# Performance work log

Measured on AMD Instinct MI355X. Metric: run time of the kernel, lower is better.

Reference implementation:

```python
import jax, jax.numpy as jnp
import numpy as np

S = 1024      # MAX_SEQ_LEN
D_IN = 4096
H = 32        # num_heads
G = 8         # num_kv_groups
HD = 128      # head_dim
GS = H // G   # group_size


def _rope(t, cos, sin):
    # t: [heads, S, HD]; cos/sin: [S, HD]
    half = HD // 2
    t1, t2 = t[..., :half], t[..., half:]
    rotated = jnp.concatenate([-t2, t1], axis=-1)
    return t * cos[None] + rotated * sin[None]


def setup_inputs() -> dict:
    key = jax.random.key(0)
    ks = jax.random.split(key, 8)
    x = jax.random.normal(ks[0], (1, S, D_IN), dtype=jnp.float32)
    mask = jnp.triu(jnp.ones((S, S), dtype=bool), k=1)  # causal: True above diagonal
    # RoPE tables (standard llama frequencies)
    inv_freq = 1.0 / (10000.0 ** (jnp.arange(0, HD, 2, dtype=jnp.float32) / HD))
    angles = jnp.arange(S, dtype=jnp.float32)[:, None] * inv_freq[None, :]  # [S, HD/2]
    angles = jnp.concatenate([angles, angles], axis=-1)                     # [S, HD]
    cos, sin = jnp.cos(angles), jnp.sin(angles)
    sc = 0.02
    Wq = jax.random.normal(ks[1], (D_IN, H * HD), dtype=jnp.float32) * sc
    Wk = jax.random.normal(ks[2], (D_IN, G * HD), dtype=jnp.float32) * sc
    Wv = jax.random.normal(ks[3], (D_IN, G * HD), dtype=jnp.float32) * sc
    Wo = jax.random.normal(ks[4], (H * HD, D_IN), dtype=jnp.float32) * sc
    return {"x": x, "mask": mask, "cos": cos, "sin": sin,
            "Wq": Wq, "Wk": Wk, "Wv": Wv, "Wo": Wo}


def reference(x, mask, cos, sin, Wq, Wk, Wv, Wo):
    b, n_tok, _ = x.shape  # b == 1 (module squeezes dim 0)
    xs = x[0]                                        # [S, d_in]
    q = (xs @ Wq).reshape(n_tok, H, HD).transpose(1, 0, 2)   # [H, S, HD]
    k = (xs @ Wk).reshape(n_tok, G, HD).transpose(1, 0, 2)   # [G, S, HD]
    v = (xs @ Wv).reshape(n_tok, G, HD).transpose(1, 0, 2)   # [G, S, HD]
    q = _rope(q, cos, sin)
    k = _rope(k, cos, sin)
    # GQA expansion: repeat_interleave over head dim
    k = jnp.repeat(k, GS, axis=0)                    # [H, S, HD]
    v = jnp.repeat(v, GS, axis=0)
    scores = jnp.einsum('hsd,htd->hst', q, k)        # [H, S, S]
    scores = jnp.where(mask[None], -jnp.inf, scores) / jnp.sqrt(jnp.float32(HD))
    weights = jax.nn.softmax(scores, axis=-1)
    ctx = jnp.einsum('hst,htd->hsd', weights, v)     # [H, S, HD]
    ctx = ctx.transpose(1, 0, 2).reshape(n_tok, H * HD)
    out = ctx @ Wo                                   # [S, d_in]
    return out[None]                                 # [1, S, d_in]
```

## Files before the change

### kernel.cpp

```cpp
#include <hip/hip_runtime.h>
#include <hip/hip_bf16.h>

#define S_LEN 1024
#define DIN 4096
#define NH 32
#define NG 8
#define HD 128

typedef __bf16 bf16x8 __attribute__((ext_vector_type(8)));
typedef __bf16 bf16x4 __attribute__((ext_vector_type(4)));
typedef float f32x4 __attribute__((ext_vector_type(4)));

__device__ __forceinline__ void gload_lds16(const void* g, void* l) {
  __builtin_amdgcn_global_load_lds(
      (const __attribute__((address_space(1))) unsigned int*)g,
      (__attribute__((address_space(3))) unsigned int*)l, 16, 0, 0);
}

__device__ __forceinline__ unsigned pack2bf(float a, float b) {
  union { __bf16 h[2]; unsigned u; } x;
  x.h[0] = (__bf16)a; x.h[1] = (__bf16)b;
  return x.u;
}

__global__ __launch_bounds__(256) void k_cast(const float* __restrict__ in,
                                              __bf16* __restrict__ out, int n4) {
  int i = blockIdx.x * 256 + threadIdx.x;
  if (i >= n4) return;
  const float4 v = ((const float4*)in)[i];
  bf16x4 o;
  o.x = (__bf16)v.x; o.y = (__bf16)v.y; o.z = (__bf16)v.z; o.w = (__bf16)v.w;
  ((bf16x4*)out)[i] = o;
}

__global__ __launch_bounds__(256) void k_transpose_cast(const float* __restrict__ W,
                                                        __bf16* __restrict__ WT,
                                                        int N, int K) {
  __shared__ __bf16 t[64][80];
  const int tid = threadIdx.x;
  const int k0 = blockIdx.y * 64, n0 = blockIdx.x * 64;
#pragma unroll
  for (int p = 0; p < 4; ++p) {
    int kk = p * 16 + (tid >> 4);
    int nn = (tid & 15) * 4;
    const float4 v = *(const float4*)&W[(size_t)(k0 + kk) * N + n0 + nn];
    t[nn + 0][kk] = (__bf16)v.x;
    t[nn + 1][kk] = (__bf16)v.y;
    t[nn + 2][kk] = (__bf16)v.z;
    t[nn + 3][kk] = (__bf16)v.w;
  }
  __syncthreads();
#pragma unroll
  for (int p = 0; p < 2; ++p) {
    int nn = p * 32 + (tid >> 3);
    int kk = (tid & 7) * 8;
    bf16x8 v = *(const bf16x8*)&t[nn][kk];
    *(bf16x8*)&WT[(size_t)(n0 + nn) * K + k0 + kk] = v;
  }
}

__global__ __launch_bounds__(256) void k_rope(__bf16* __restrict__ Q, __bf16* __restrict__ Kb,
                                              const float* __restrict__ cosT,
                                              const float* __restrict__ sinT) {
  int idx = blockIdx.x * 256 + threadIdx.x;
  const int QP = S_LEN * NH * 64;
  __bf16* t; int nh;
  if (idx < QP) { t = Q; nh = NH; }
  else {
    idx -= QP; t = Kb; nh = NG;
    if (idx >= S_LEN * NG * 64) return;
  }
  int d = idx & 63;
  int h = (idx >> 6) % nh;
  int s = idx / (64 * nh);
  float c = cosT[s * HD + d], sn = sinT[s * HD + d];
  size_t base = (size_t)s * nh * HD + h * HD + d;
  float t1 = (float)t[base], t2 = (float)t[base + 64];
  t[base]      = (__bf16)(t1 * c - t2 * sn);
  t[base + 64] = (__bf16)(t2 * c + t1 * sn);
}

__global__ __launch_bounds__(256) void k_vt(const __bf16* __restrict__ V,
                                            __bf16* __restrict__ Vt) {
  __shared__ __bf16 t[64][72];
  const int tid = threadIdx.x;
  const int s0 = blockIdx.y * 64, d0 = blockIdx.x * 64;
#pragma unroll
  for (int p = 0; p < 2; ++p) {
    int ss = p * 32 + (tid >> 3);
    int dd = (tid & 7) * 8;
    bf16x8 v = *(const bf16x8*)&V[(size_t)(s0 + ss) * 1024 + d0 + dd];
#pragma unroll
    for (int e = 0; e < 8; ++e) t[dd + e][ss] = v[e];
  }
  __syncthreads();
#pragma unroll
  for (int p = 0; p < 2; ++p) {
    int dd = p * 32 + (tid >> 3);
    int ss = (tid & 7) * 8;
    *(bf16x8*)&Vt[(size_t)(d0 + dd) * 1024 + s0 + ss] = *(const bf16x8*)&t[dd][ss];
  }
}

template <int MODE, typename OutT>
__global__ __launch_bounds__(256, 3) void k_gemm(const __bf16* __restrict__ A,
                                                 const __bf16* __restrict__ Bt,
                                                 OutT* __restrict__ C, int N, int K,
                                                 __bf16* __restrict__ Qb,
                                                 __bf16* __restrict__ Kb,
                                                 __bf16* __restrict__ Vb) {
  __shared__ __bf16 As[128 * 64], Bs[64 * 64];
  const int bm = blockIdx.y, bn = blockIdx.x;
  const int tid = threadIdx.x, w = tid >> 6;
  const int l = tid & 63, l15 = l & 15, g4 = l >> 4;

  f32x4 acc[2][4];
#pragma unroll
  for (int i = 0; i < 2; ++i)
#pragma unroll
    for (int j = 0; j < 4; ++j)
#pragma unroll
      for (int r = 0; r < 4; ++r) acc[i][j][r] = 0.f;

  for (int k0 = 0; k0 < K; k0 += 64) {
#pragma unroll
    for (int p = 0; p < 4; ++p) {
      int c = p * 256 + tid;
      int row = c >> 3, gc = (c & 7) ^ (row & 7);
      gload_lds16(&A[(size_t)(bm * 128 + row) * K + k0 + gc * 8], &As[(p * 256 + w * 64) * 8]);
    }
#pragma unroll
    for (int p = 0; p < 2; ++p) {
      int c = p * 256 + tid;
      int row = c >> 3, gc = (c & 7) ^ (row & 7);
      gload_lds16(&Bt[(size_t)(bn * 64 + row) * K + k0 + gc * 8], &Bs[(p * 256 + w * 64) * 8]);
    }
    __syncthreads();

    bf16x8 af[2][2], bfr[4][2];
#pragma unroll
    for (int i = 0; i < 2; ++i) {
      int m = w * 32 + i * 16 + l15;
#pragma unroll
      for (int kk = 0; kk < 2; ++kk)
        af[i][kk] = *(const bf16x8*)((const char*)As + m * 128 + (((kk * 4 + g4) ^ (m & 7)) << 4));
    }
#pragma unroll
    for (int j = 0; j < 4; ++j) {
      int n = j * 16 + l15;
#pragma unroll
      for (int kk = 0; kk < 2; ++kk)
        bfr[j][kk] = *(const bf16x8*)((const char*)Bs + n * 128 + (((kk * 4 + g4) ^ (n & 7)) << 4));
    }
#pragma unroll
    for (int kk = 0; kk < 2; ++kk)
#pragma unroll
      for (int i = 0; i < 2; ++i)
#pragma unroll
        for (int j = 0; j < 4; ++j)
          acc[i][j] = __builtin_amdgcn_mfma_f32_16x16x32_bf16(af[i][kk], bfr[j][kk], acc[i][j], 0, 0, 0);
    __syncthreads();
  }

  if constexpr (MODE == 0) {
#pragma unroll
    for (int i = 0; i < 2; ++i)
#pragma unroll
      for (int j = 0; j < 4; ++j)
#pragma unroll
        for (int r = 0; r < 4; ++r) {
          size_t row = bm * 128 + w * 32 + i * 16 + g4 * 4 + r;
          size_t col = bn * 64 + j * 16 + l15;
          C[row * N + col] = (OutT)acc[i][j][r];
        }
  } else {
    const int nb0 = bn * 64;
    __bf16* dst; int ldc, coff;
    if (nb0 < 4096)      { dst = Qb; ldc = 4096; coff = 0; }
    else if (nb0 < 5120) { dst = Kb; ldc = 1024; coff = 4096; }
    else                 { dst = Vb; ldc = 1024; coff = 5120; }
#pragma unroll
    for (int i = 0; i < 2; ++i)
#pragma unroll
      for (int j = 0; j < 4; ++j)
#pragma unroll
        for (int r = 0; r < 4; ++r) {
          size_t row = bm * 128 + w * 32 + i * 16 + g4 * 4 + r;
          size_t col = nb0 + j * 16 + l15 - coff;
          dst[row * ldc + col] = (__bf16)acc[i][j][r];
        }
  }
}

__global__ __launch_bounds__(256) void k_attn(const __bf16* __restrict__ Q,
                                              const __bf16* __restrict__ Kb,
                                              const __bf16* __restrict__ Vt,
                                              __bf16* __restrict__ ctx) {
  __shared__ __align__(16) char lds_raw[65536];
  __bf16* Ks = (__bf16*)lds_raw;
  __bf16* Vs = (__bf16*)(lds_raw + 32768);

  const int h = blockIdx.y, g = h >> 2;
  const int q0 = blockIdx.x * 64;
  const int tid = threadIdx.x, w = tid >> 6, l = tid & 63;
  const int l15 = l & 15, g4 = l >> 4;
  const float scale = 0.08838834764831845f;

  bf16x8 qf[4];
  const int qrow = q0 + w * 16 + l15;
#pragma unroll
  for (int ks = 0; ks < 4; ++ks)
    qf[ks] = *(const bf16x8*)&Q[(size_t)qrow * (NH * HD) + h * HD + ks * 32 + g4 * 8];

  f32x4 acc[8];
#pragma unroll
  for (int i = 0; i < 8; ++i)
#pragma unroll
    for (int r = 0; r < 4; ++r) acc[i][r] = 0.f;
  float m_run = -__builtin_inff(), l_run = 0.f;

  const int ntiles = (q0 + 64 + 127) >> 7;
  for (int kt = 0; kt < ntiles; ++kt) {
    const int kv0 = kt * 128;
#pragma unroll
    for (int p = 0; p < 8; ++p) {
      int c = p * 256 + tid;
      int row = c >> 4, cc = c & 15;
      gload_lds16(&Kb[(size_t)(kv0 + row) * (NG * HD) + g * HD + ((cc ^ (row & 7)) << 3)],
                  &Ks[(p * 256 + w * 64) * 8]);
      gload_lds16(&Vt[(size_t)(g * HD + row) * S_LEN + kv0 + ((cc ^ (row & 7)) << 3)],
                  &Vs[(p * 256 + w * 64) * 8]);
    }
    __syncthreads();

    float sreg[8][4];
    const bool need_mask = (kv0 + 127 > q0);
#pragma unroll
    for (int tf = 0; tf < 8; ++tf) {
      f32x4 sa;
#pragma unroll
      for (int r = 0; r < 4; ++r) sa[r] = 0.f;
      int t_loc = tf * 16 + l15;
#pragma unroll
      for (int ks = 0; ks < 4; ++ks) {
        bf16x8 kf = *(const bf16x8*)((const char*)Ks + t_loc * 256 + (((ks * 4 + g4) ^ (t_loc & 7)) << 4));
        sa = __builtin_amdgcn_mfma_f32_16x16x32_bf16(kf, qf[ks], sa, 0, 0, 0);
      }
#pragma unroll
      for (int r = 0; r < 4; ++r) {
        float v = sa[r] * scale;
        if (need_mask && (kv0 + tf * 16 + g4 * 4 + r) > qrow) v = -__builtin_inff();
        sreg[tf][r] = v;
      }
    }
    float mx = -__builtin_inff();
#pragma unroll
    for (int tf = 0; tf < 8; ++tf)
#pragma unroll
      for (int r = 0; r < 4; ++r) mx = fmaxf(mx, sreg[tf][r]);
    mx = fmaxf(mx, __shfl_xor(mx, 16));
    mx = fmaxf(mx, __shfl_xor(mx, 32));
    const float m_new = fmaxf(m_run, mx);
    const float alpha = __expf(m_run - m_new);
    float ssum = 0.f;
#pragma unroll
    for (int tf = 0; tf < 8; ++tf)
#pragma unroll
      for (int r = 0; r < 4; ++r) {
        sreg[tf][r] = __expf(sreg[tf][r] - m_new);
        ssum += sreg[tf][r];
      }
    ssum += __shfl_xor(ssum, 16);
    ssum += __shfl_xor(ssum, 32);
    l_run = l_run * alpha + ssum;
    m_run = m_new;
    float ar[4];
#pragma unroll
    for (int r = 0; r < 4; ++r) ar[r] = __shfl(alpha, g4 * 4 + r);
#pragma unroll
    for (int nf = 0; nf < 8; ++nf)
#pragma unroll
      for (int r = 0; r < 4; ++r) acc[nf][r] *= ar[r];

    __syncthreads();

    char* pb = lds_raw + w * 4096;
#pragma unroll
    for (int tf = 0; tf < 8; ++tf) {
      int chunkc = 2 * tf + (g4 >> 1);
      int addr = l15 * 256 + ((chunkc ^ (l15 & 7)) << 4) + ((g4 & 1) << 3);
      *(unsigned*)(pb + addr)     = pack2bf(sreg[tf][0], sreg[tf][1]);
      *(unsigned*)(pb + addr + 4) = pack2bf(sreg[tf][2], sreg[tf][3]);
    }
    asm volatile("s_waitcnt lgkmcnt(0)" ::: "memory");
    bf16x8 pf[4];
#pragma unroll
    for (int ks = 0; ks < 4; ++ks)
      pf[ks] = *(const bf16x8*)(pb + l15 * 256 + (((ks * 4 + g4) ^ (l15 & 7)) << 4));
#pragma unroll
    for (int nf = 0; nf < 8; ++nf) {
      int d_loc = nf * 16 + l15;
#pragma unroll
      for (int ks = 0; ks < 4; ++ks) {
        bf16x8 vf = *(const bf16x8*)((const char*)Vs + d_loc * 256 + (((ks * 4 + g4) ^ (d_loc & 7)) << 4));
        acc[nf] = __builtin_amdgcn_mfma_f32_16x16x32_bf16(pf[ks], vf, acc[nf], 0, 0, 0);
      }
    }
    __syncthreads();
  }
  float li[4];
#pragma unroll
  for (int r = 0; r < 4; ++r) li[r] = 1.f / __shfl(l_run, g4 * 4 + r);
#pragma unroll
  for (int nf = 0; nf < 8; ++nf)
#pragma unroll
    for (int r = 0; r < 4; ++r) {
      size_t row = q0 + w * 16 + g4 * 4 + r;
      size_t col = (size_t)h * HD + nf * 16 + l15;
      ctx[row * (NH * HD) + col] = (__bf16)(acc[nf][r] * li[r]);
    }
}

extern "C" void kernel_launch(void* const* d_in, const int* in_sizes, int n_in,
                              void* d_out, int out_size, void* d_ws, size_t ws_size,
                              hipStream_t stream) {
  const float* x    = (const float*)d_in[0];
  const float* cosT = (const float*)d_in[2];
  const float* sinT = (const float*)d_in[3];
  const float* Wq   = (const float*)d_in[4];
  const float* Wk   = (const float*)d_in[5];
  const float* Wv   = (const float*)d_in[6];
  const float* Wo   = (const float*)d_in[7];
  float* out = (float*)d_out;

  char* ws = (char*)d_ws;
  const size_t MB = 1u << 20;
  __bf16* xb    = (__bf16*)(ws + 0);
  __bf16* WqkvT = (__bf16*)(ws + 8 * MB);
  __bf16* WoT   = (__bf16*)(ws + 56 * MB);
  __bf16* Qb    = (__bf16*)(ws + 88 * MB);
  __bf16* Kbuf  = (__bf16*)(ws + 96 * MB);
  __bf16* Vb    = (__bf16*)(ws + 98 * MB);
  __bf16* Vtb   = (__bf16*)(ws + 100 * MB);
  __bf16* ctxb  = (__bf16*)(ws + 0);

  k_cast<<<4096, 256, 0, stream>>>(x, xb, (S_LEN * DIN) / 4);
  k_transpose_cast<<<dim3(64, 64), 256, 0, stream>>>(Wq, WqkvT, 4096, 4096);
  k_transpose_cast<<<dim3(16, 64), 256, 0, stream>>>(Wk, WqkvT + (size_t)4096 * 4096, 1024, 4096);
  k_transpose_cast<<<dim3(16, 64), 256, 0, stream>>>(Wv, WqkvT + (size_t)5120 * 4096, 1024, 4096);
  k_transpose_cast<<<dim3(64, 64), 256, 0, stream>>>(Wo, WoT, 4096, 4096);

  k_gemm<1, __bf16><<<dim3(96, 8), 256, 0, stream>>>(xb, WqkvT, (__bf16*)nullptr, 6144, 4096,
                                                     Qb, Kbuf, Vb);
  k_rope<<<10240, 256, 0, stream>>>(Qb, Kbuf, cosT, sinT);
  k_vt<<<dim3(16, 16), 256, 0, stream>>>(Vb, Vtb);

  k_attn<<<dim3(16, 32), 256, 0, stream>>>(Qb, Kbuf, Vtb, ctxb);

  k_gemm<0, float><<<dim3(64, 8), 256, 0, stream>>>(ctxb, WoT, out, 4096, 4096,
                                                    nullptr, nullptr, nullptr);
}
```

Baseline: 223.2 us.

## Merge prep kernels, double-buffer GEMM LDS, fuse V transpose, vectorize RoPE

Folds the x cast and the four weight transpose-casts into one launch, and double-buffers the GEMM's LDS tiles so the next K-tile loads while the current one is computed. The QKV GEMM epilogue writes V straight into transposed layout, which removes the separate transpose kernel. RoPE now processes four elements per thread with vector loads. Together these cut launch count and exposed load latency, at the cost of twice the LDS per GEMM block, which may lower occupancy.

```diff
diff --git a/kernel.cpp b/kernel.cpp
--- a/kernel.cpp
+++ b/kernel.cpp
@@ -23,22 +23,33 @@
   return x.u;
 }
 
-__global__ __launch_bounds__(256) void k_cast(const float* __restrict__ in,
-                                              __bf16* __restrict__ out, int n4) {
-  int i = blockIdx.x * 256 + threadIdx.x;
-  if (i >= n4) return;
-  const float4 v = ((const float4*)in)[i];
-  bf16x4 o;
-  o.x = (__bf16)v.x; o.y = (__bf16)v.y; o.z = (__bf16)v.z; o.w = (__bf16)v.w;
-  ((bf16x4*)out)[i] = o;
-}
-
-__global__ __launch_bounds__(256) void k_transpose_cast(const float* __restrict__ W,
-                                                        __bf16* __restrict__ WT,
-                                                        int N, int K) {
+__global__ __launch_bounds__(256) void k_prep(const float* __restrict__ x,
+                                              const float* __restrict__ Wq,
+                                              const float* __restrict__ Wk,
+                                              const float* __restrict__ Wv,
+                                              const float* __restrict__ Wo,
+                                              __bf16* __restrict__ xb,
+                                              __bf16* __restrict__ WqkvT,
+                                              __bf16* __restrict__ WoT) {
   __shared__ __bf16 t[64][80];
   const int tid = threadIdx.x;
-  const int k0 = blockIdx.y * 64, n0 = blockIdx.x * 64;
+  int bid = blockIdx.x;
+  if (bid < 4096) {
+    int i = bid * 256 + tid;
+    const float4 v = ((const float4*)x)[i];
+    bf16x4 o;
+    o.x = (__bf16)v.x; o.y = (__bf16)v.y; o.z = (__bf16)v.z; o.w = (__bf16)v.w;
+    ((bf16x4*)xb)[i] = o;
+    return;
+  }
+  bid -= 4096;
+  const float* W; __bf16* WT; int N, off, tau;
+  if (bid < 4096)       { W = Wq; WT = WqkvT; N = 4096; off = 0;    tau = bid; }
+  else if (bid < 5120)  { W = Wk; WT = WqkvT; N = 1024; off = 4096; tau = bid - 4096; }
+  else if (bid < 6144)  { W = Wv; WT = WqkvT; N = 1024; off = 5120; tau = bid - 5120; }
+  else                  { W = Wo; WT = WoT;   N = 4096; off = 0;    tau = bid - 6144; }
+  const int ntx = N >> 6;
+  const int n0 = (tau % ntx) * 64, k0 = (tau / ntx) * 64;
 #pragma unroll
   for (int p = 0; p < 4; ++p) {
     int kk = p * 16 + (tid >> 4);
@@ -55,7 +66,7 @@
     int nn = p * 32 + (tid >> 3);
     int kk = (tid & 7) * 8;
     bf16x8 v = *(const bf16x8*)&t[nn][kk];
-    *(bf16x8*)&WT[(size_t)(n0 + nn) * K + k0 + kk] = v;
+    *(bf16x8*)&WT[(size_t)(off + n0 + nn) * DIN + k0 + kk] = v;
   }
 }
 
@@ -63,57 +74,46 @@
                                               const float* __restrict__ cosT,
                                               const float* __restrict__ sinT) {
   int idx = blockIdx.x * 256 + threadIdx.x;
-  const int QP = S_LEN * NH * 64;
-  __bf16* t; int nh;
-  if (idx < QP) { t = Q; nh = NH; }
-  else {
-    idx -= QP; t = Kb; nh = NG;
-    if (idx >= S_LEN * NG * 64) return;
-  }
-  int d = idx & 63;
-  int h = (idx >> 6) % nh;
-  int s = idx / (64 * nh);
-  float c = cosT[s * HD + d], sn = sinT[s * HD + d];
-  size_t base = (size_t)s * nh * HD + h * HD + d;
-  float t1 = (float)t[base], t2 = (float)t[base + 64];
-  t[base]      = (__bf16)(t1 * c - t2 * sn);
-  t[base + 64] = (__bf16)(t2 * c + t1 * sn);
-}
-
-__global__ __launch_bounds__(256) void k_vt(const __bf16* __restrict__ V,
-                                            __bf16* __restrict__ Vt) {
-  __shared__ __bf16 t[64][72];
-  const int tid = threadIdx.x;
-  const int s0 = blockIdx.y * 64, d0 = blockIdx.x * 64;
-#pragma unroll
-  for (int p = 0; p < 2; ++p) {
-    int ss = p * 32 + (tid >> 3);
-    int dd = (tid & 7) * 8;
-    bf16x8 v = *(const bf16x8*)&V[(size_t)(s0 + ss) * 1024 + d0 + dd];
-#pragma unroll
-    for (int e = 0; e < 8; ++e) t[dd + e][ss] = v[e];
-  }
-  __syncthreads();
-#pragma unroll
-  for (int p = 0; p < 2; ++p) {
-    int dd = p * 32 + (tid >> 3);
-    int ss = (tid & 7) * 8;
-    *(bf16x8*)&Vt[(size_t)(d0 + dd) * 1024 + s0 + ss] = *(const bf16x8*)&t[dd][ss];
-  }
-}
-
-template <int MODE, typename OutT>
+  int d = (idx & 15) * 4;
+  int row = idx >> 4;
+  __bf16* p; int s;
+  if (row < S_LEN * NH) { p = Q + (size_t)row * HD; s = row >> 5; }
+  else { int r = row - S_LEN * NH; p = Kb + (size_t)r * HD; s = r >> 3; }
+  const float4 c = *(const float4*)&cosT[s * HD + d];
+  const float4 sn = *(const float4*)&sinT[s * HD + d];
+  bf16x4 a = *(const bf16x4*)&p[d];
+  bf16x4 b = *(const bf16x4*)&p[d + 64];
+  bf16x4 oa, ob;
+  oa.x = (__bf16)((float)a.x * c.x - (float)b.x * sn.x);
+  oa.y = (__bf16)((float)a.y * c.y - (float)b.y * sn.y);
+  oa.z = (__bf16)((float)a.z * c.z - (float)b.z * sn.z);
+  oa.w = (__bf16)((float)a.w * c.w - (float)b.w * sn.w);
+  ob.x = (__bf16)((float)b.x * c.x + (float)a.x * sn.x);
+  ob.y = (__bf16)((float)b.y * c.y + (float)a.y * sn.y);
+  ob.z = (__bf16)((float)b.z * c.z + (float)a.z * sn.z);
+  ob.w = (__bf16)((float)b.w * c.w + (float)a.w * sn.w);
+  *(bf16x4*)&p[d] = oa;
+  *(bf16x4*)&p[d + 64] = ob;
+}
+
+template <int MODE>
 __global__ __launch_bounds__(256, 3) void k_gemm(const __bf16* __restrict__ A,
                                                  const __bf16* __restrict__ Bt,
-                                                 OutT* __restrict__ C, int N, int K,
+                                                 float* __restrict__ C,
                                                  __bf16* __restrict__ Qb,
                                                  __bf16* __restrict__ Kb,
-                                                 __bf16* __restrict__ Vb) {
-  __shared__ __bf16 As[128 * 64], Bs[64 * 64];
+                                                 __bf16* __restrict__ Vt) {
+  __shared__ __bf16 As[2][128 * 64];
+  __shared__ __bf16 Bs[2][64 * 64];
   const int bm = blockIdx.y, bn = blockIdx.x;
+  const int K = DIN, NT = K / 64;
+
   const int tid = threadIdx.x, w = tid >> 6;
   const int l = tid & 63, l15 = l & 15, g4 = l >> 4;
 
+  const __bf16* Asrc = A + (size_t)(bm * 128) * K;
+  const __bf16* Bsrc = Bt + (size_t)(bn * 64) * K;
+
   f32x4 acc[2][4];
 #pragma unroll
   for (int i = 0; i < 2; ++i)
@@ -122,35 +122,37 @@
 #pragma unroll
       for (int r = 0; r < 4; ++r) acc[i][j][r] = 0.f;
 
-  for (int k0 = 0; k0 < K; k0 += 64) {
+  auto issueA = [&](int t, __bf16* dst) {
 #pragma unroll
     for (int p = 0; p < 4; ++p) {
       int c = p * 256 + tid;
       int row = c >> 3, gc = (c & 7) ^ (row & 7);
-      gload_lds16(&A[(size_t)(bm * 128 + row) * K + k0 + gc * 8], &As[(p * 256 + w * 64) * 8]);
-    }
+      gload_lds16(Asrc + (size_t)row * K + t * 64 + gc * 8, dst + (p * 256 + w * 64) * 8);
+    }
+  };
+  auto issueB = [&](int t, __bf16* dst) {
 #pragma unroll
     for (int p = 0; p < 2; ++p) {
       int c = p * 256 + tid;
       int row = c >> 3, gc = (c & 7) ^ (row & 7);
-      gload_lds16(&Bt[(size_t)(bn * 64 + row) * K + k0 + gc * 8], &Bs[(p * 256 + w * 64) * 8]);
-    }
-    __syncthreads();
-
+      gload_lds16(Bsrc + (size_t)row * K + t * 64 + gc * 8, dst + (p * 256 + w * 64) * 8);
+    }
+  };
+  auto compute = [&](const __bf16* Ab, const __bf16* Bb) {
     bf16x8 af[2][2], bfr[4][2];
 #pragma unroll
     for (int i = 0; i < 2; ++i) {
       int m = w * 32 + i * 16 + l15;
 #pragma unroll
       for (int kk = 0; kk < 2; ++kk)
-        af[i][kk] = *(const bf16x8*)((const char*)As + m * 128 + (((kk * 4 + g4) ^ (m & 7)) << 4));
+        af[i][kk] = *(const bf16x8*)((const char*)Ab + m * 128 + (((kk * 4 + g4) ^ (m & 7)) << 4));
     }
 #pragma unroll
     for (int j = 0; j < 4; ++j) {
       int n = j * 16 + l15;
 #pragma unroll
       for (int kk = 0; kk < 2; ++kk)
-        bfr[j][kk] = *(const bf16x8*)((const char*)Bs + n * 128 + (((kk * 4 + g4) ^ (n & 7)) << 4));
+        bfr[j][kk] = *(const bf16x8*)((const char*)Bb + n * 128 + (((kk * 4 + g4) ^ (n & 7)) << 4));
     }
 #pragma unroll
     for (int kk = 0; kk < 2; ++kk)
@@ -159,6 +161,17 @@
 #pragma unroll
         for (int j = 0; j < 4; ++j)
           acc[i][j] = __builtin_amdgcn_mfma_f32_16x16x32_bf16(af[i][kk], bfr[j][kk], acc[i][j], 0, 0, 0);
+  };
+
+  issueA(0, As[0]); issueB(0, Bs[0]);
+  __syncthreads();
+
+  for (int t = 0; t < NT; t += 2) {
+    issueA(t + 1, As[1]); issueB(t + 1, Bs[1]);
+    compute(As[0], Bs[0]);
+    __syncthreads();
+    if (t + 2 < NT) { issueA(t + 2, As[0]); issueB(t + 2, Bs[0]); }
+    compute(As[1], Bs[1]);
     __syncthreads();
   }
 
@@ -171,24 +184,37 @@
         for (int r = 0; r < 4; ++r) {
           size_t row = bm * 128 + w * 32 + i * 16 + g4 * 4 + r;
           size_t col = bn * 64 + j * 16 + l15;
-          C[row * N + col] = (OutT)acc[i][j][r];
+          C[row * 4096 + col] = acc[i][j][r];
         }
   } else {
     const int nb0 = bn * 64;
-    __bf16* dst; int ldc, coff;
-    if (nb0 < 4096)      { dst = Qb; ldc = 4096; coff = 0; }
-    else if (nb0 < 5120) { dst = Kb; ldc = 1024; coff = 4096; }
-    else                 { dst = Vb; ldc = 1024; coff = 5120; }
-#pragma unroll
-    for (int i = 0; i < 2; ++i)
-#pragma unroll
-      for (int j = 0; j < 4; ++j)
-#pragma unroll
-        for (int r = 0; r < 4; ++r) {
-          size_t row = bm * 128 + w * 32 + i * 16 + g4 * 4 + r;
-          size_t col = nb0 + j * 16 + l15 - coff;
-          dst[row * ldc + col] = (__bf16)acc[i][j][r];
+    if (bn < 80) {
+      __bf16* dst = (bn < 64) ? Qb : Kb;
+      int ldc = (bn < 64) ? 4096 : 1024;
+      int coff = (bn < 64) ? 0 : 4096;
+#pragma unroll
+      for (int i = 0; i < 2; ++i)
+#pragma unroll
+        for (int j = 0; j < 4; ++j)
+#pragma unroll
+          for (int r = 0; r < 4; ++r) {
+            size_t row = bm * 128 + w * 32 + i * 16 + g4 * 4 + r;
+            size_t col = nb0 - coff + j * 16 + l15;
+            dst[row * ldc + col] = (__bf16)acc[i][j][r];
+          }
+    } else {
+#pragma unroll
+      for (int i = 0; i < 2; ++i)
+#pragma unroll
+        for (int j = 0; j < 4; ++j) {
+          size_t n = nb0 - 5120 + j * 16 + l15;
+          size_t m0 = bm * 128 + w * 32 + i * 16 + g4 * 4;
+          bf16x4 v;
+          v.x = (__bf16)acc[i][j][0]; v.y = (__bf16)acc[i][j][1];
+          v.z = (__bf16)acc[i][j][2]; v.w = (__bf16)acc[i][j][3];
+          *(bf16x4*)&Vt[n * 1024 + m0] = v;
         }
+    }
   }
 }
 
@@ -340,23 +366,16 @@
   __bf16* WoT   = (__bf16*)(ws + 56 * MB);
   __bf16* Qb    = (__bf16*)(ws + 88 * MB);
   __bf16* Kbuf  = (__bf16*)(ws + 96 * MB);
-  __bf16* Vb    = (__bf16*)(ws + 98 * MB);
-  __bf16* Vtb   = (__bf16*)(ws + 100 * MB);
+  __bf16* Vtb   = (__bf16*)(ws + 98 * MB);
   __bf16* ctxb  = (__bf16*)(ws + 0);
 
-  k_cast<<<4096, 256, 0, stream>>>(x, xb, (S_LEN * DIN) / 4);
-  k_transpose_cast<<<dim3(64, 64), 256, 0, stream>>>(Wq, WqkvT, 4096, 4096);
-  k_transpose_cast<<<dim3(16, 64), 256, 0, stream>>>(Wk, WqkvT + (size_t)4096 * 4096, 1024, 4096);
-  k_transpose_cast<<<dim3(16, 64), 256, 0, stream>>>(Wv, WqkvT + (size_t)5120 * 4096, 1024, 4096);
-  k_transpose_cast<<<dim3(64, 64), 256, 0, stream>>>(Wo, WoT, 4096, 4096);
-
-  k_gemm<1, __bf16><<<dim3(96, 8), 256, 0, stream>>>(xb, WqkvT, (__bf16*)nullptr, 6144, 4096,
-                                                     Qb, Kbuf, Vb);
-  k_rope<<<10240, 256, 0, stream>>>(Qb, Kbuf, cosT, sinT);
-  k_vt<<<dim3(16, 16), 256, 0, stream>>>(Vb, Vtb);
+  k_prep<<<14336, 256, 0, stream>>>(x, Wq, Wk, Wv, Wo, xb, WqkvT, WoT);
+
+  k_gemm<1><<<dim3(96, 8), 256, 0, stream>>>(xb, WqkvT, nullptr, Qb, Kbuf, Vtb);
+
+  k_rope<<<2560, 256, 0, stream>>>(Qb, Kbuf, cosT, sinT);
 
   k_attn<<<dim3(16, 32), 256, 0, stream>>>(Qb, Kbuf, Vtb, ctxb);
 
-  k_gemm<0, float><<<dim3(64, 8), 256, 0, stream>>>(ctxb, WoT, out, 4096, 4096,
-                                                    nullptr, nullptr, nullptr);
-}
+  k_gemm<0><<<dim3(64, 8), 256, 0, stream>>>(ctxb, WoT, out, nullptr, nullptr, nullptr);
+}
```

Result: faster. 214.6 us (-3.9%).
